# Performance work log

Hardware: AMD Instinct MI355X
Metric: run time of the kernel (lower is better)

Reference implementation:

```python
import jax, jax.numpy as jnp
import numpy as np

B, C, H, W = 4, 3, 1024, 1024
EPS = 1e-8


def setup_inputs() -> dict:
    key = jax.random.key(0)
    k1, k2 = jax.random.split(key)
    im0 = jax.random.normal(k1, (B, C, H, W), dtype=jnp.float32)
    # grid = identity pixel mesh + small random water-distortion displacement
    yy, xx = jnp.meshgrid(jnp.arange(H, dtype=jnp.float32),
                          jnp.arange(W, dtype=jnp.float32), indexing='ij')
    base = jnp.stack([xx, yy], axis=-1)  # [H,W,2] in (x,y) order
    disp = 2.0 * jax.random.normal(k2, (B, H, W, 2), dtype=jnp.float32)
    grid = base[None] + disp  # [B,H,W,2]
    return {"im0": im0, "grid": grid}


def reference(im0, grid):
    """Forward splatting (griddata): scatter im0 values at coordinates `grid`
    onto the regular HxW grid with bilinear weights, normalized by the
    accumulated weight at each cell."""
    b, c, h, w = im0.shape
    n = h * w
    x = grid[..., 0].reshape(b, n)
    y = grid[..., 1].reshape(b, n)
    x0f = jnp.floor(x)
    y0f = jnp.floor(y)
    dx = x - x0f  # bilinear fractions (differentiable w.r.t. grid)
    dy = y - y0f
    x0 = x0f.astype(jnp.int32)
    y0 = y0f.astype(jnp.int32)

    # 4 corner indices [b,4,n] and bilinear weights
    xs = jnp.stack([x0, x0 + 1, x0, x0 + 1], axis=1)
    ys = jnp.stack([y0, y0, y0 + 1, y0 + 1], axis=1)
    ws = jnp.stack([(1 - dx) * (1 - dy), dx * (1 - dy),
                    (1 - dx) * dy, dx * dy], axis=1)
    valid = (xs >= 0) & (xs < w) & (ys >= 0) & (ys < h)
    ws = ws * valid.astype(ws.dtype)
    idx = (jnp.clip(ys, 0, h - 1) * w + jnp.clip(xs, 0, w - 1)).reshape(b, 4 * n)
    ws = ws.reshape(b, 4 * n)

    vals = im0.reshape(b, c, n)
    contrib = (vals[:, :, None, :] * ws.reshape(b, 1, 4, n)).reshape(b, c, 4 * n)

    def splat(v, wgt, i):
        den = jnp.zeros((n,), wgt.dtype).at[i].add(wgt)
        num = jnp.zeros((c, n), v.dtype).at[:, i].add(v)
        return num / jnp.maximum(den, EPS)[None, :]

    out = jax.vmap(splat)(contrib, ws, idx)  # [b,c,n]
    return out.reshape(b, c, h, w)
```

## Files before the change

kernel.cpp:

```cpp
#include <hip/hip_runtime.h>
#include <hip/hip_fp16.h>

#define B 4
#define C 3
#define H 1024
#define W 1024
#define N (H * W)
#define EPS 1e-8f

#define TW 32
#define TH 32
#define R 8
#define WIN 48
#define NSRC (WIN * WIN)
#define NTASKS (NSRC / 4)
#define BDIM 33
#define NBINS (BDIM * BDIM)
#define NBINW ((NBINS + 1) / 2)
#define NTX (W / TW)
#define NTY (H / TH)
#define NTILES (NTX * NTY * B)

struct OutlierRec { int idx; float dw, d0, d1, d2; };

__global__ __launch_bounds__(256, 6) void splat_gather(
    const float* __restrict__ im0,
    const float* __restrict__ grid,
    float* __restrict__ out,
    float* __restrict__ den,
    int* __restrict__ tileCnt,
    OutlierRec* __restrict__ recs,
    int slots)
{
    __shared__ unsigned recW0[NSRC];
    __shared__ unsigned recW1[NSRC];
    __shared__ unsigned short recV2[NSRC];
    __shared__ unsigned binCntP[NBINW];
    __shared__ int wtot[4];

    const int bid = blockIdx.x;
    const int b = bid >> 10;
    const int t = bid & 1023;
    const int tx0 = (t & (NTX - 1)) * TW;
    const int ty0 = (t >> 5) * TH;
    const int tid = threadIdx.x;

    for (int i = tid; i < NBINW; i += 256) binCntP[i] = 0u;
    __syncthreads();

    const int lx0 = tx0 - R;
    const int ly0 = ty0 - R;

    const float* imb   = im0 + (size_t)b * C * N;
    const float* gbase = grid + (size_t)b * N * 2;

    auto push_rec = [&](int xi, int yi, float w, float v0, float v1, float v2) {
        const int tile = (b << 10) | ((yi >> 5) << 5) | (xi >> 5);
        const int slot = atomicAdd(&tileCnt[tile], 1);
        if (slot < slots) {
            OutlierRec r;
            r.idx = b * N + yi * W + xi;
            r.dw = w; r.d0 = v0 * w; r.d1 = v1 * w; r.d2 = v2 * w;
            recs[(size_t)tile * slots + slot] = r;
        }
    };

    for (int task = tid; task < NTASKS; task += 256) {
        const int row = task / (WIN / 4);
        const int col = (task - row * (WIN / 4)) * 4;
        const int sy = ly0 + row;
        const int sxg = lx0 + col;
        if ((unsigned)sy >= H || (unsigned)sxg >= W) continue;

        const int n = sy * W + sxg;
        const float4 g0 = *(const float4*)(gbase + 2 * n);
        const float4 g1 = *(const float4*)(gbase + 2 * n + 4);
        const float gxk[4] = {g0.x, g0.z, g1.x, g1.z};
        const float gyk[4] = {g0.y, g0.w, g1.y, g1.w};
#pragma unroll
        for (int k = 0; k < 4; ++k) {
            const int x0 = (int)floorf(gxk[k]);
            const int y0 = (int)floorf(gyk[k]);
            const int bx = x0 - tx0 + 1;
            const int by = y0 - ty0 + 1;
            if ((unsigned)bx < BDIM && (unsigned)by < BDIM) {
                const int bin = by * BDIM + bx;
                atomicAdd(&binCntP[bin >> 1], 1u << ((unsigned)(bin & 1) * 16u));
            }
        }
    }
    __syncthreads();

    {
        int c[6] = {0, 0, 0, 0, 0, 0};
        const int w0 = tid * 3;
        const bool act = (tid * 6) < NBINS;
        if (act) {
#pragma unroll
            for (int j = 0; j < 3; ++j) {
                const int w = w0 + j;
                const unsigned wv = (w < NBINW) ? binCntP[w] : 0u;
                c[2 * j]     = (int)(wv & 0xffffu);
                c[2 * j + 1] = (int)(wv >> 16);
            }
        }
        const int tsum = c[0] + c[1] + c[2] + c[3] + c[4] + c[5];
        int x = tsum;
#pragma unroll
        for (int off = 1; off < 64; off <<= 1) {
            const int y = __shfl_up(x, off);
            if ((tid & 63) >= off) x += y;
        }
        if ((tid & 63) == 63) wtot[tid >> 6] = x;
        __syncthreads();
        int ex = x - tsum;
        for (int i = 0; i < (tid >> 6); ++i) ex += wtot[i];
        if (act) {
#pragma unroll
            for (int j = 0; j < 3; ++j) {
                const int w = w0 + j;
                if (w < NBINW) {
                    const unsigned lo = (unsigned)ex; ex += c[2 * j];
                    const unsigned hi = (unsigned)ex; ex += c[2 * j + 1];
                    binCntP[w] = (lo & 0xffffu) | (hi << 16);
                }
            }
        }
    }
    __syncthreads();

    for (int task = tid; task < NTASKS; task += 256) {
        const int row = task / (WIN / 4);
        const int col = (task - row * (WIN / 4)) * 4;
        const int sy = ly0 + row;
        const int sxg = lx0 + col;
        if ((unsigned)sy >= H || (unsigned)sxg >= W) continue;

        const int n = sy * W + sxg;
        const float4 g0 = *(const float4*)(gbase + 2 * n);
        const float4 g1 = *(const float4*)(gbase + 2 * n + 4);
        const float4 c0 = *(const float4*)(imb + n);
        const float4 c1 = *(const float4*)(imb + N + n);
        const float4 c2 = *(const float4*)(imb + 2 * N + n);

        const float gxk[4] = {g0.x, g0.z, g1.x, g1.z};
        const float gyk[4] = {g0.y, g0.w, g1.y, g1.w};
        const float v0k[4] = {c0.x, c0.y, c0.z, c0.w};
        const float v1k[4] = {c1.x, c1.y, c1.z, c1.w};
        const float v2k[4] = {c2.x, c2.y, c2.z, c2.w};

#pragma unroll
        for (int k = 0; k < 4; ++k) {
            const int sx = sxg + k;
            const float gx = gxk[k], gy = gyk[k];
            const float x0f = floorf(gx);
            const float y0f = floorf(gy);
            const float dx = gx - x0f;
            const float dy = gy - y0f;
            const int x0 = (int)x0f;
            const int y0 = (int)y0f;

            const int bx = x0 - tx0 + 1;
            const int by = y0 - ty0 + 1;
            if ((unsigned)bx < BDIM && (unsigned)by < BDIM) {
                const int bin = by * BDIM + bx;
                const unsigned sh = (unsigned)(bin & 1) * 16u;
                const unsigned old = atomicAdd(&binCntP[bin >> 1], 1u << sh);
                const int slot = (int)((old >> sh) & 0xffffu);
                unsigned dq = (unsigned)(dx * 65536.0f);
                unsigned eq = (unsigned)(dy * 65536.0f);
                if (dq > 65535u) dq = 65535u;
                if (eq > 65535u) eq = 65535u;
                recW0[slot] = dq | (eq << 16);
                __half2 h01 = __floats2half2_rn(v0k[k], v1k[k]);
                recW1[slot] = *(unsigned*)&h01;
                recV2[slot] = __half_as_ushort(__float2half_rn(v2k[k]));
            }

            if ((unsigned)(sx - tx0) < TW && (unsigned)(sy - ty0) < TH) {
                const float wxa[2] = {1.f - dx, dx};
                const float wya[2] = {1.f - dy, dy};
#pragma unroll
                for (int cy2 = 0; cy2 < 2; ++cy2)
#pragma unroll
                    for (int cx2 = 0; cx2 < 2; ++cx2) {
                        const int xi = x0 + cx2, yi = y0 + cy2;
                        if ((unsigned)xi < W && (unsigned)yi < H) {
                            const int ox0 = (xi >> 5) << 5;
                            const int oy0 = (yi >> 5) << 5;
                            const bool covered =
                                (sx >= ox0 - R) && (sx < ox0 + TW + R) &&
                                (sy >= oy0 - R) && (sy < oy0 + TH + R);
                            if (!covered)
                                push_rec(xi, yi, wxa[cx2] * wya[cy2],
                                         v0k[k], v1k[k], v2k[k]);
                        }
                    }
            }
        }
    }
    __syncthreads();

    const int cx = tid & 31;
    const int ry = (tid >> 5) * 4;
    float* outb = out + (size_t)b * C * N;
    float* denb = den + (size_t)b * N;

    auto END = [&](int bb) -> int {
        const unsigned wv = binCntP[bb >> 1];
        return (int)((wv >> ((unsigned)(bb & 1) * 16u)) & 0xffffu);
    };

    float d[4]  = {0.f, 0.f, 0.f, 0.f};
    float a0[4] = {0.f, 0.f, 0.f, 0.f};
    float a1[4] = {0.f, 0.f, 0.f, 0.f};
    float a2[4] = {0.f, 0.f, 0.f, 0.f};

#pragma unroll
    for (int s = 0; s < 5; ++s) {
        const int by = ry + s;
        const int bin0 = by * BDIM + cx;
        const int e0 = (bin0 == 0) ? 0 : END(bin0 - 1);
        const int m  = END(bin0);
        const int e1 = END(bin0 + 1);
        for (int e = e0; e < e1; ++e) {
            const unsigned w0 = recW0[e];
            const unsigned uv01 = recW1[e];
            const float dx = (float)(w0 & 0xffffu) * (1.f / 65536.f);
            const float dy = (float)(w0 >> 16) * (1.f / 65536.f);
            const float2 v01 = __half22float2(*(const __half2*)&uv01);
            const float v2 = __half2float(__ushort_as_half(recV2[e]));
            const float wx = (e < m) ? dx : (1.f - dx);
            if (s > 0) {
                const float w = wx * (1.f - dy);
                d[s - 1] += w;
                a0[s - 1] += v01.x * w;
                a1[s - 1] += v01.y * w;
                a2[s - 1] += v2 * w;
            }
            if (s < 4) {
                const float w = wx * dy;
                d[s] += w;
                a0[s] += v01.x * w;
                a1[s] += v01.y * w;
                a2[s] += v2 * w;
            }
        }
    }

#pragma unroll
    for (int s = 0; s < 4; ++s) {
        const float inv = 1.f / fmaxf(d[s], EPS);
        const int gi = (ty0 + ry + s) * W + tx0 + cx;
        denb[gi] = d[s];
        outb[gi]         = a0[s] * inv;
        outb[N + gi]     = a1[s] * inv;
        outb[2 * N + gi] = a2[s] * inv;
    }
}

__global__ __launch_bounds__(64) void fix_tiles(
    float* __restrict__ out,
    float* __restrict__ den,
    const int* __restrict__ tileCnt,
    const OutlierRec* __restrict__ recs,
    int slots)
{
    const int bid = blockIdx.x;
    int cnt = tileCnt[bid];
    if (cnt <= 0) return;
    cnt = min(cnt, slots);
    const int tid = threadIdx.x;
    if (tid >= cnt) return;

    OutlierRec rec = recs[(size_t)bid * slots + tid];
    float dw = rec.dw, d0 = rec.d0, d1 = rec.d1, d2 = rec.d2;
    bool first = true;
    for (int r2 = 0; r2 < cnt; ++r2) {
        if (r2 == tid) continue;
        OutlierRec o = recs[(size_t)bid * slots + r2];
        if (o.idx == rec.idx) {
            if (r2 < tid) { first = false; break; }
            dw += o.dw; d0 += o.d0; d1 += o.d1; d2 += o.d2;
        }
    }
    if (!first) return;

    const int b = rec.idx >> 20;
    const int cell = rec.idx & (N - 1);
    float* outb = out + (size_t)b * C * N + cell;
    float* dptr = den + ((size_t)b << 20) + cell;

    float d = *dptr;
    const float m = fmaxf(d, EPS);
    float n0 = outb[0] * m;
    float n1 = outb[N] * m;
    float n2 = outb[2 * N] * m;
    d += dw; n0 += d0; n1 += d1; n2 += d2;
    const float inv = 1.f / fmaxf(d, EPS);
    *dptr = d;
    outb[0]     = n0 * inv;
    outb[N]     = n1 * inv;
    outb[2 * N] = n2 * inv;
}

extern "C" void kernel_launch(void* const* d_in, const int* in_sizes, int n_in,
                              void* d_out, int out_size, void* d_ws, size_t ws_size,
                              hipStream_t stream) {
    const float* im0 = (const float*)d_in[0];
    const float* grid = (const float*)d_in[1];
    float* out = (float*)d_out;

    int* tileCnt = (int*)d_ws;
    float* den = (float*)((char*)d_ws + 16384);
    const size_t rec_off = 16384 + (size_t)B * N * sizeof(float);
    OutlierRec* recs = (OutlierRec*)((char*)d_ws + rec_off);
    int slots = 0;
    if (ws_size > rec_off) {
        size_t avail = (ws_size - rec_off) / sizeof(OutlierRec);
        slots = (int)(avail / NTILES);
        if (slots > 32) slots = 32;
    }

    (void)hipMemsetAsync(tileCnt, 0, NTILES * sizeof(int), stream);

    splat_gather<<<NTILES, 256, 0, stream>>>(im0, grid, out, den,
                                             tileCnt, recs, slots);
    fix_tiles<<<NTILES, 64, 0, stream>>>(out, den, tileCnt, recs, slots);
}
```

Measured before the change: 160.2 us.

## Cache grid-derived bin info in registers, shrink shared record buffers with overflow spill

The grid is now read once per tile: the first pass stores quantized fractions, bin index and an outlier flag in registers, and the second pass reloads only image values. It skips the image loads for tasks with no in-window points. Shared record arrays are cut to NREC entries, and records past that limit go to the global outlier list. The smaller shared footprint allows a higher launch-bounds occupancy target (8 blocks). Register pressure rises, and overflow records take a slower global atomic path.

```diff
diff --git a/kernel.cpp b/kernel.cpp
--- a/kernel.cpp
+++ b/kernel.cpp
@@ -14,16 +14,18 @@
 #define WIN 48
 #define NSRC (WIN * WIN)
 #define NTASKS (NSRC / 4)
+#define COLG (WIN / 4)
 #define BDIM 33
 #define NBINS (BDIM * BDIM)
 #define NBINW ((NBINS + 1) / 2)
+#define NREC 1536
 #define NTX (W / TW)
 #define NTY (H / TH)
 #define NTILES (NTX * NTY * B)
 
 struct OutlierRec { int idx; float dw, d0, d1, d2; };
 
-__global__ __launch_bounds__(256, 6) void splat_gather(
+__global__ __launch_bounds__(256, 8) void splat_gather(
     const float* __restrict__ im0,
     const float* __restrict__ grid,
     float* __restrict__ out,
@@ -32,9 +34,9 @@
     OutlierRec* __restrict__ recs,
     int slots)
 {
-    __shared__ unsigned recW0[NSRC];
-    __shared__ unsigned recW1[NSRC];
-    __shared__ unsigned short recV2[NSRC];
+    __shared__ unsigned recW0[NREC];
+    __shared__ unsigned recW1[NREC];
+    __shared__ unsigned short recV2[NREC];
     __shared__ unsigned binCntP[NBINW];
     __shared__ int wtot[4];
 
@@ -65,9 +67,16 @@
         }
     };
 
-    for (int task = tid; task < NTASKS; task += 256) {
-        const int row = task / (WIN / 4);
-        const int col = (task - row * (WIN / 4)) * 4;
+    unsigned cw[3][4];
+    unsigned cbp[3][2];
+
+#pragma unroll
+    for (int it = 0; it < 3; ++it) {
+        cbp[it][0] = 0u; cbp[it][1] = 0u;
+        if (it == 2 && tid >= NTASKS - 512) continue;
+        const int task = tid + it * 256;
+        const int row = task / COLG;
+        const int col = (task - row * COLG) * 4;
         const int sy = ly0 + row;
         const int sxg = lx0 + col;
         if ((unsigned)sy >= H || (unsigned)sxg >= W) continue;
@@ -77,78 +86,8 @@
         const float4 g1 = *(const float4*)(gbase + 2 * n + 4);
         const float gxk[4] = {g0.x, g0.z, g1.x, g1.z};
         const float gyk[4] = {g0.y, g0.w, g1.y, g1.w};
-#pragma unroll
-        for (int k = 0; k < 4; ++k) {
-            const int x0 = (int)floorf(gxk[k]);
-            const int y0 = (int)floorf(gyk[k]);
-            const int bx = x0 - tx0 + 1;
-            const int by = y0 - ty0 + 1;
-            if ((unsigned)bx < BDIM && (unsigned)by < BDIM) {
-                const int bin = by * BDIM + bx;
-                atomicAdd(&binCntP[bin >> 1], 1u << ((unsigned)(bin & 1) * 16u));
-            }
-        }
-    }
-    __syncthreads();
-
-    {
-        int c[6] = {0, 0, 0, 0, 0, 0};
-        const int w0 = tid * 3;
-        const bool act = (tid * 6) < NBINS;
-        if (act) {
-#pragma unroll
-            for (int j = 0; j < 3; ++j) {
-                const int w = w0 + j;
-                const unsigned wv = (w < NBINW) ? binCntP[w] : 0u;
-                c[2 * j]     = (int)(wv & 0xffffu);
-                c[2 * j + 1] = (int)(wv >> 16);
-            }
-        }
-        const int tsum = c[0] + c[1] + c[2] + c[3] + c[4] + c[5];
-        int x = tsum;
-#pragma unroll
-        for (int off = 1; off < 64; off <<= 1) {
-            const int y = __shfl_up(x, off);
-            if ((tid & 63) >= off) x += y;
-        }
-        if ((tid & 63) == 63) wtot[tid >> 6] = x;
-        __syncthreads();
-        int ex = x - tsum;
-        for (int i = 0; i < (tid >> 6); ++i) ex += wtot[i];
-        if (act) {
-#pragma unroll
-            for (int j = 0; j < 3; ++j) {
-                const int w = w0 + j;
-                if (w < NBINW) {
-                    const unsigned lo = (unsigned)ex; ex += c[2 * j];
-                    const unsigned hi = (unsigned)ex; ex += c[2 * j + 1];
-                    binCntP[w] = (lo & 0xffffu) | (hi << 16);
-                }
-            }
-        }
-    }
-    __syncthreads();
-
-    for (int task = tid; task < NTASKS; task += 256) {
-        const int row = task / (WIN / 4);
-        const int col = (task - row * (WIN / 4)) * 4;
-        const int sy = ly0 + row;
-        const int sxg = lx0 + col;
-        if ((unsigned)sy >= H || (unsigned)sxg >= W) continue;
-
-        const int n = sy * W + sxg;
-        const float4 g0 = *(const float4*)(gbase + 2 * n);
-        const float4 g1 = *(const float4*)(gbase + 2 * n + 4);
-        const float4 c0 = *(const float4*)(imb + n);
-        const float4 c1 = *(const float4*)(imb + N + n);
-        const float4 c2 = *(const float4*)(imb + 2 * N + n);
-
-        const float gxk[4] = {g0.x, g0.z, g1.x, g1.z};
-        const float gyk[4] = {g0.y, g0.w, g1.y, g1.w};
-        const float v0k[4] = {c0.x, c0.y, c0.z, c0.w};
-        const float v1k[4] = {c1.x, c1.y, c1.z, c1.w};
-        const float v2k[4] = {c2.x, c2.y, c2.z, c2.w};
-
+
+        unsigned cv[4];
 #pragma unroll
         for (int k = 0; k < 4; ++k) {
             const int sx = sxg + k;
@@ -160,24 +99,148 @@
             const int x0 = (int)x0f;
             const int y0 = (int)y0f;
 
+            unsigned dq = (unsigned)(dx * 65536.0f);
+            unsigned eq = (unsigned)(dy * 65536.0f);
+            if (dq > 65535u) dq = 65535u;
+            if (eq > 65535u) eq = 65535u;
+            cw[it][k] = dq | (eq << 16);
+
+            unsigned c = 0u;
             const int bx = x0 - tx0 + 1;
             const int by = y0 - ty0 + 1;
             if ((unsigned)bx < BDIM && (unsigned)by < BDIM) {
                 const int bin = by * BDIM + bx;
+                atomicAdd(&binCntP[bin >> 1],
+                          1u << ((unsigned)(bin & 1) * 16u));
+                c = (unsigned)(bin + 1);
+            }
+            if ((unsigned)(sx - tx0) < TW && (unsigned)(sy - ty0) < TH) {
+                if (!(fabsf(gx - (float)sx) <= 6.f &&
+                      fabsf(gy - (float)sy) <= 6.f)) {
+                    bool outl = false;
+#pragma unroll
+                    for (int cy2 = 0; cy2 < 2; ++cy2)
+#pragma unroll
+                        for (int cx2 = 0; cx2 < 2; ++cx2) {
+                            const int xi = x0 + cx2, yi = y0 + cy2;
+                            if ((unsigned)xi < W && (unsigned)yi < H) {
+                                const int ox0 = (xi >> 5) << 5;
+                                const int oy0 = (yi >> 5) << 5;
+                                if (sx < ox0 - R || sx >= ox0 + TW + R ||
+                                    sy < oy0 - R || sy >= oy0 + TH + R)
+                                    outl = true;
+                            }
+                        }
+                    if (outl) c |= 0x8000u;
+                }
+            }
+            cv[k] = c;
+        }
+        cbp[it][0] = cv[0] | (cv[1] << 16);
+        cbp[it][1] = cv[2] | (cv[3] << 16);
+    }
+    __syncthreads();
+
+    {
+        int c[6] = {0, 0, 0, 0, 0, 0};
+        const int w0 = tid * 3;
+        const bool act = (tid * 6) < NBINS;
+        if (act) {
+#pragma unroll
+            for (int j = 0; j < 3; ++j) {
+                const int w = w0 + j;
+                const unsigned wv = (w < NBINW) ? binCntP[w] : 0u;
+                c[2 * j]     = (int)(wv & 0xffffu);
+                c[2 * j + 1] = (int)(wv >> 16);
+            }
+        }
+        const int tsum = c[0] + c[1] + c[2] + c[3] + c[4] + c[5];
+        int x = tsum;
+#pragma unroll
+        for (int off = 1; off < 64; off <<= 1) {
+            const int y = __shfl_up(x, off);
+            if ((tid & 63) >= off) x += y;
+        }
+        if ((tid & 63) == 63) wtot[tid >> 6] = x;
+        __syncthreads();
+        int ex = x - tsum;
+        for (int i = 0; i < (tid >> 6); ++i) ex += wtot[i];
+        if (act) {
+#pragma unroll
+            for (int j = 0; j < 3; ++j) {
+                const int w = w0 + j;
+                if (w < NBINW) {
+                    const unsigned lo = (unsigned)ex; ex += c[2 * j];
+                    const unsigned hi = (unsigned)ex; ex += c[2 * j + 1];
+                    binCntP[w] = (lo & 0xffffu) | (hi << 16);
+                }
+            }
+        }
+    }
+    __syncthreads();
+
+#pragma unroll
+    for (int it = 0; it < 3; ++it) {
+        if (it == 2 && tid >= NTASKS - 512) continue;
+        const unsigned p0 = cbp[it][0], p1 = cbp[it][1];
+        if (!(p0 | p1)) continue;
+        const int task = tid + it * 256;
+        const int row = task / COLG;
+        const int col = (task - row * COLG) * 4;
+        const int sy = ly0 + row;
+        const int sxg = lx0 + col;
+        const int n = sy * W + sxg;
+        const float4 c0 = *(const float4*)(imb + n);
+        const float4 c1 = *(const float4*)(imb + N + n);
+        const float4 c2 = *(const float4*)(imb + 2 * N + n);
+        const float v0k[4] = {c0.x, c0.y, c0.z, c0.w};
+        const float v1k[4] = {c1.x, c1.y, c1.z, c1.w};
+        const float v2k[4] = {c2.x, c2.y, c2.z, c2.w};
+
+#pragma unroll
+        for (int k = 0; k < 4; ++k) {
+            const unsigned cv = (((k & 2) ? p1 : p0) >> ((k & 1) * 16)) & 0xffffu;
+            const unsigned binp1 = cv & 0x7fffu;
+            if (binp1) {
+                const int bin = (int)binp1 - 1;
                 const unsigned sh = (unsigned)(bin & 1) * 16u;
                 const unsigned old = atomicAdd(&binCntP[bin >> 1], 1u << sh);
                 const int slot = (int)((old >> sh) & 0xffffu);
-                unsigned dq = (unsigned)(dx * 65536.0f);
-                unsigned eq = (unsigned)(dy * 65536.0f);
-                if (dq > 65535u) dq = 65535u;
-                if (eq > 65535u) eq = 65535u;
-                recW0[slot] = dq | (eq << 16);
-                __half2 h01 = __floats2half2_rn(v0k[k], v1k[k]);
-                recW1[slot] = *(unsigned*)&h01;
-                recV2[slot] = __half_as_ushort(__float2half_rn(v2k[k]));
-            }
-
-            if ((unsigned)(sx - tx0) < TW && (unsigned)(sy - ty0) < TH) {
+                const unsigned w0 = cw[it][k];
+                if (slot < NREC) {
+                    recW0[slot] = w0;
+                    __half2 h01 = __floats2half2_rn(v0k[k], v1k[k]);
+                    recW1[slot] = *(unsigned*)&h01;
+                    recV2[slot] = __half_as_ushort(__float2half_rn(v2k[k]));
+                } else {
+                    const float dx = (float)(w0 & 0xffffu) * (1.f / 65536.f);
+                    const float dy = (float)(w0 >> 16) * (1.f / 65536.f);
+                    const int x0 = tx0 - 1 + bin % BDIM;
+                    const int y0 = ty0 - 1 + bin / BDIM;
+                    const float wxa[2] = {1.f - dx, dx};
+                    const float wya[2] = {1.f - dy, dy};
+#pragma unroll
+                    for (int cy2 = 0; cy2 < 2; ++cy2)
+#pragma unroll
+                        for (int cx2 = 0; cx2 < 2; ++cx2) {
+                            const int xi = x0 + cx2, yi = y0 + cy2;
+                            if ((unsigned)(xi - tx0) < TW &&
+                                (unsigned)(yi - ty0) < TH)
+                                push_rec(xi, yi, wxa[cx2] * wya[cy2],
+                                         v0k[k], v1k[k], v2k[k]);
+                        }
+                }
+            }
+            if (cv & 0x8000u) {
+                const int sx = sxg + k;
+                const float gx = gbase[2 * (n + k)];
+                const float gy = gbase[2 * (n + k) + 1];
+                const float x0f = floorf(gx);
+                const float y0f = floorf(gy);
+                const float dx = gx - x0f;
+                const float dy = gy - y0f;
+                const int x0 = (int)x0f;
+                const int y0 = (int)y0f;
                 const float wxa[2] = {1.f - dx, dx};
                 const float wya[2] = {1.f - dy, dy};
 #pragma unroll
@@ -220,9 +283,10 @@
     for (int s = 0; s < 5; ++s) {
         const int by = ry + s;
         const int bin0 = by * BDIM + cx;
-        const int e0 = (bin0 == 0) ? 0 : END(bin0 - 1);
-        const int m  = END(bin0);
-        const int e1 = END(bin0 + 1);
+        int e0 = (bin0 == 0) ? 0 : END(bin0 - 1);
+        int m  = END(bin0);
+        int e1 = END(bin0 + 1);
+        e0 = min(e0, NREC); m = min(m, NREC); e1 = min(e1, NREC);
         for (int e = e0; e < e1; ++e) {
             const unsigned w0 = recW0[e];
             const unsigned uv01 = recW1[e];
```

Measured after the change: 147.4 us. 1.09x faster.
